# Kernel optimization log

Measured on AMD Instinct MI355X. Metric: run time of the kernel, lower is better.

## Reference

```python
import jax, jax.numpy as jnp
import numpy as np

DT = 0.5
NE, NIN = 400, 784
# excitatory LIF
THRESH_E, OFFSET, VRESET_E, EREST_E, REFRAC_E, TAU_MEM_E = -52.0, 20.0, -65.0, -65.0, 5.0, 100.0
# inhibitory LIF
THRESH_I, VRESET_I, EREST_I, REFRAC_I, TAU_MEM_I = -40.0, -45.0, -60.0, 2.0, 10.0
# synapses
TAU_SYN_E, TAU_SYN_I = 1.0, 2.0
E_EI, E_IE, E_EE = 0.0, -100.0, 0.0
# STDP
TC_P1, TC_P2, TC_PRE = 20.0, 40.0, 20.0
NU_PRE, NU_POST, WMAX = 0.0001, 0.01, 1.0
THETA0 = 20.0


def lif_step(mem, rc, I, thresh, v_reset, erest, tau, refrac):
    # conductance-based LIF with refractory period (inferred LIFei semantics)
    active = rc <= 0.0
    mem = jnp.where(active, mem + (erest - mem + I) * (DT / tau), mem)
    rc = jnp.maximum(rc - DT, 0.0)
    spike = (active & (mem > thresh)).astype(mem.dtype)
    fired = spike > 0.0
    mem = jnp.where(fired, v_reset, mem)
    rc = jnp.where(fired, refrac, rc)
    return mem, rc, spike


def setup_inputs() -> dict:
    key = jax.random.key(0)
    k1, k2 = jax.random.split(key)
    x = jax.random.uniform(k1, (50, 512, NIN), dtype=jnp.float32)  # Poisson-rate encoded frames
    W_ine = (jax.random.uniform(k2, (NE, NIN), dtype=jnp.float32) + 0.01) * 0.3  # create_ine
    W_ei = jnp.eye(NE, dtype=jnp.float32) * 10.4                                  # create_ei
    W_ie = (jnp.ones((NE, NE), jnp.float32) - jnp.eye(NE, dtype=jnp.float32)) * 17.0  # create_ie
    return {"x": x, "W_ine": W_ine, "W_ei": W_ei, "W_ie": W_ie}


def reference(x, W_ine, W_ei, W_ie):
    T, B, _ = x.shape
    z_e = jnp.zeros((B, NE), x.dtype)

    def step(carry, xt_t):
        xt, t = xt_t
        (W, g_ine, g_ei, g_ie, Iie, mem_e, rc_e, mem_i, rc_i,
         theta, tr_pre, tp1, tp2) = carry
        # normweight: rows sum to 78.4
        W = W / (jnp.sum(W, axis=1, keepdims=True) / 78.4)
        # input -> e synapse (STDP-plastic)
        dg_ine = xt @ W.T                         # (B, NE)
        I_ine = g_ine * (E_EE - mem_e)            # g=0 at t=0 -> I=0 (matches None init)
        g_ine = g_ine + (dg_ine - g_ine) * (DT / TAU_SYN_E)
        # excitatory LIF with adaptive threshold
        thr_e = THRESH_E - OFFSET + theta
        mem_e, rc_e, spike_e = lif_step(mem_e, rc_e, I_ine + Iie, thr_e,
                                        VRESET_E, EREST_E, TAU_MEM_E, REFRAC_E)
        # e -> i synapse
        dg_ei = spike_e @ W_ei.T
        I_ei = g_ei * (E_EI - mem_i)
        g_ei = g_ei + (dg_ei - g_ei) * (DT / TAU_SYN_E)
        # inhibitory LIF
        mem_i, rc_i, spike_i = lif_step(mem_i, rc_i, I_ei, THRESH_I,
                                        VRESET_I, EREST_I, TAU_MEM_I, REFRAC_I)
        # i -> e synapse (current fed into NEXT step's lif_e)
        dg_ie = spike_i @ W_ie.T
        Iie = g_ie * (E_IE - mem_e)
        g_ie = g_ie + (dg_ie - g_ie) * (DT / TAU_SYN_I)
        # threshold homeostasis
        theta = theta * (1.0 - DT / 1e7) + 0.05 * spike_e
        # pre trace: first call copies x, later decay then set to 1 where x>0.9
        tr_pre_upd = jnp.where(xt > 0.9, 1.0, tr_pre * (1.0 - DT / TC_PRE))
        tr_pre = jnp.where(t == 0, xt, tr_pre_upd)
        # post traces: return decayed value, then set to 1 where spike
        ret1 = tp1 * (1.0 - DT / TC_P1)
        ret2 = tp2 * (1.0 - DT / TC_P2)
        fired = spike_e > 0.9
        tp1 = jnp.where(fired, 1.0, ret1)
        tp2 = jnp.where(fired, 1.0, ret2)
        # STDP: autograd.grad of dg=x@W^T w.r.t. W with grad_outputs G is G^T @ x
        dw = (NU_PRE * jnp.einsum('be,bi->ei', ret1, xt)
              + NU_POST * jnp.einsum('be,bi->ei', spike_e * ret2, tr_pre))
        W = jnp.clip(W + dw, 0.0, WMAX)
        new_carry = (W, g_ine, g_ei, g_ie, Iie, mem_e, rc_e, mem_i, rc_i,
                     theta, tr_pre, tp1, tp2)
        return new_carry, spike_e

    carry0 = (W_ine,
              z_e, z_e, z_e,                      # g_ine, g_ei, g_ie
              z_e,                                # Iie
              jnp.full((B, NE), EREST_E, x.dtype), z_e,   # mem_e, rc_e
              jnp.full((B, NE), EREST_I, x.dtype), z_e,   # mem_i, rc_i
              jnp.full((B, NE), THETA0, x.dtype),         # theta
              jnp.zeros((B, NIN), x.dtype),               # trace_pre
              z_e, z_e)                                   # trace_post1/2
    _, spikes = jax.lax.scan(step, carry0, (x, jnp.arange(T)))
    return spikes  # (T, B, NE)
```

## Files before the change

kernel.cpp:

```cpp
#include <hip/hip_runtime.h>

#define NE 400
#define NIN 784
#define BB 512
#define TT 50

#define KC1 14
#define KCH1 56
#define KT1 8
#define KC2 16
#define KCH2 64

constexpr float C_KE     = (float)(0.5 / 100.0);
constexpr float C_KI     = (float)(0.5 / 10.0);
constexpr float C_GSE    = 0.5f;
constexpr float C_GSI    = 0.25f;
constexpr float C_DECTH  = (float)(1.0 - 0.5 / 1e7);
constexpr float C_DEC1   = (float)(1.0 - 0.5 / 20.0);
constexpr float C_DEC2   = (float)(1.0 - 0.5 / 40.0);
constexpr float C_DECPRE = (float)(1.0 - 0.5 / 20.0);
constexpr float C_NUPRE  = (float)0.0001;
constexpr float C_NUPOST = 0.01f;

__global__ void k_init(float* g_ine, float* g_ei, float* g_ie, float* Iie,
                       float* mem_e, float* rc_e, float* mem_i, float* rc_i,
                       float* theta, float* tp1, float* tp2) {
    int i = blockIdx.x * blockDim.x + threadIdx.x;
    if (i < BB * NE) {
        g_ine[i] = 0.f; g_ei[i] = 0.f; g_ie[i] = 0.f; Iie[i] = 0.f;
        mem_e[i] = -65.0f; rc_e[i] = 0.f;
        mem_i[i] = -60.0f; rc_i[i] = 0.f;
        theta[i] = 20.0f; tp1[i] = 0.f; tp2[i] = 0.f;
    }
}

__global__ __launch_bounds__(256) void k_pre(const float* __restrict__ W,
                                             float* __restrict__ d,
                                             const float* __restrict__ x0,
                                             float* __restrict__ tr) {
    int bid = blockIdx.x, tid = threadIdx.x;
    if (bid >= NE) {
        int base = (bid - NE) * 2048 + tid * 4;
        *(float4*)&tr[base] = *(const float4*)&x0[base];
        return;
    }
    __shared__ float red[256];
    float s = 0.f;
    if (tid < 196) {
        float4 w = *(const float4*)&W[bid * NIN + tid * 4];
        s = w.x + w.y + w.z + w.w;
    }
    red[tid] = s;
    __syncthreads();
    for (int off = 128; off > 0; off >>= 1) {
        if (tid < off) red[tid] += red[tid + off];
        __syncthreads();
    }
    if (tid == 0) d[bid] = red[0] / 78.4f;
}

__global__ __launch_bounds__(256) void k_g1(const float* __restrict__ x,
                                            const float* __restrict__ W,
                                            float* __restrict__ dgp) {
    __shared__ float sA[KT1][68];
    __shared__ float sB[KT1][132];
    const int lid = threadIdx.x;
    const int tx = lid & 15, ty = lid >> 4;
    const int e0 = blockIdx.x * 128, b0 = blockIdx.y * 64;
    const int kb = blockIdx.z * KCH1;
    const int xr = lid >> 2, xc = (lid & 3) * 2;
    const int wr = lid >> 1, wc = (lid & 1) * 4;
    const bool wv_ok = (e0 + wr) < NE;
    const float4 z4 = make_float4(0.f, 0.f, 0.f, 0.f);

    float acc[4][2][4];
#pragma unroll
    for (int p = 0; p < 4; p++)
#pragma unroll
        for (int h = 0; h < 2; h++)
#pragma unroll
            for (int q = 0; q < 4; q++) acc[p][h][q] = 0.f;

    float2 xv;
    float4 wv;
    auto ld = [&](int kt) {
        int k0 = kb + kt * KT1;
        xv = *(const float2*)&x[(b0 + xr) * NIN + k0 + xc];
        wv = wv_ok ? *(const float4*)&W[(e0 + wr) * NIN + k0 + wc] : z4;
    };

    ld(0);
    for (int kt = 0; kt < KCH1 / KT1; kt++) {
        sA[xc + 0][xr] = xv.x; sA[xc + 1][xr] = xv.y;
        sB[wc + 0][wr] = wv.x; sB[wc + 1][wr] = wv.y;
        sB[wc + 2][wr] = wv.z; sB[wc + 3][wr] = wv.w;
        __syncthreads();
        if (kt < KCH1 / KT1 - 1) ld(kt + 1);
#pragma unroll
        for (int k = 0; k < KT1; k++) {
            float4 av = *(const float4*)&sA[k][ty * 4];
            float4 b0v = *(const float4*)&sB[k][tx * 4];
            float4 b1v = *(const float4*)&sB[k][64 + tx * 4];
            float a[4] = {av.x, av.y, av.z, av.w};
            float bq0[4] = {b0v.x, b0v.y, b0v.z, b0v.w};
            float bq1[4] = {b1v.x, b1v.y, b1v.z, b1v.w};
#pragma unroll
            for (int p = 0; p < 4; p++)
#pragma unroll
                for (int q = 0; q < 4; q++) {
                    acc[p][0][q] += a[p] * bq0[q];
                    acc[p][1][q] += a[p] * bq1[q];
                }
        }
        __syncthreads();
    }
    float* basep = dgp + (size_t)blockIdx.z * BB * NE;
    int c1 = e0 + tx * 4, c2 = e0 + 64 + tx * 4;
#pragma unroll
    for (int p = 0; p < 4; p++) {
        int row = b0 + ty * 4 + p;
        if (c1 < NE)
            *(float4*)&basep[row * NE + c1] =
                make_float4(acc[p][0][0], acc[p][0][1], acc[p][0][2], acc[p][0][3]);
        if (c2 < NE)
            *(float4*)&basep[row * NE + c2] =
                make_float4(acc[p][1][0], acc[p][1][1], acc[p][1][2], acc[p][1][3]);
    }
}

__global__ __launch_bounds__(512) void k_mid(const float* __restrict__ dgp,
                                             const float* __restrict__ d,
                                             float* g_ine, float* g_ei, float* g_ie,
                                             float* Iie, float* mem_e, float* rc_e,
                                             float* mem_i, float* rc_i, float* theta,
                                             float* tp1, float* tp2,
                                             float* __restrict__ A1s,
                                             float* __restrict__ A2s,
                                             float* __restrict__ out_t) {
    int b = blockIdx.x;
    int e = threadIdx.x;
    __shared__ float red[8];
    int idx = b * NE + e;

    float spk_i = 0.f, spk_e = 0.f;
    float g1 = 0.f, me = 0.f, re = 0.f, th = 0.f, g2 = 0.f, mi = 0.f, ri = 0.f;

    if (e < NE) {
        float dg = 0.f;
#pragma unroll
        for (int c = 0; c < KC1; c++) dg += dgp[(size_t)c * BB * NE + idx];
        dg = dg / d[e];
        g1 = g_ine[idx]; me = mem_e[idx]; re = rc_e[idx];
        th = theta[idx];
        float Ii = Iie[idx];
        float I_in = g1 * (0.0f - me);
        g1 = g1 + (dg - g1) * C_GSE;
        bool act = (re <= 0.0f);
        float I = I_in + Ii;
        if (act) me = me + ((-65.0f - me) + I) * C_KE;
        re = fmaxf(re - 0.5f, 0.0f);
        float thr = -72.0f + th;
        spk_e = (act && (me > thr)) ? 1.0f : 0.0f;
        if (spk_e > 0.0f) { me = -65.0f; re = 5.0f; }
        float dgei = spk_e * 10.4f;
        g2 = g_ei[idx]; mi = mem_i[idx]; ri = rc_i[idx];
        float I_ei = g2 * (0.0f - mi);
        g2 = g2 + (dgei - g2) * C_GSE;
        bool ai = (ri <= 0.0f);
        if (ai) mi = mi + ((-60.0f - mi) + I_ei) * C_KI;
        ri = fmaxf(ri - 0.5f, 0.0f);
        spk_i = (ai && (mi > -40.0f)) ? 1.0f : 0.0f;
        if (spk_i > 0.0f) { mi = -45.0f; ri = 2.0f; }
    }
    float v = spk_i;
#pragma unroll
    for (int o = 32; o > 0; o >>= 1) v += __shfl_down(v, o, 64);
    if ((e & 63) == 0) red[e >> 6] = v;
    __syncthreads();
    float S = ((red[0] + red[1]) + (red[2] + red[3])) +
              ((red[4] + red[5]) + (red[6] + red[7]));
    if (e < NE) {
        float dgie = 17.0f * (S - spk_i);
        float g3 = g_ie[idx];
        float Iie_new = g3 * (-100.0f - me);
        g3 = g3 + (dgie - g3) * C_GSI;
        float th2 = th * C_DECTH + 0.05f * spk_e;
        float r1 = tp1[idx] * C_DEC1;
        float r2 = tp2[idx] * C_DEC2;
        bool fired = spk_e > 0.9f;
        A1s[idx] = C_NUPRE * r1;
        A2s[idx] = C_NUPOST * (spk_e * r2);
        tp1[idx] = fired ? 1.0f : r1;
        tp2[idx] = fired ? 1.0f : r2;
        g_ine[idx] = g1; g_ei[idx] = g2; g_ie[idx] = g3; Iie[idx] = Iie_new;
        mem_e[idx] = me; rc_e[idx] = re; mem_i[idx] = mi; rc_i[idx] = ri;
        theta[idx] = th2;
        out_t[idx] = spk_e;
    }
}

__global__ __launch_bounds__(256) void k_g2(const float* __restrict__ A1s,
                                            const float* __restrict__ A2s,
                                            const float* __restrict__ x,
                                            const float* __restrict__ tr,
                                            float* __restrict__ part) {
    __shared__ float sA[16][68];
    __shared__ float sB[16][132];
    const int lid = threadIdx.x;
    const int tx = lid & 15, ty = lid >> 4;
    const int e0 = blockIdx.x * 64, i0 = blockIdx.y * 128;
    const int kb = blockIdx.z * KCH2;
    const int kr = lid >> 4;
    const int jc = (lid & 15) * 4;
    const float4 z4 = make_float4(0.f, 0.f, 0.f, 0.f);

    float acc[4][2][4];
#pragma unroll
    for (int p = 0; p < 4; p++)
#pragma unroll
        for (int h = 0; h < 2; h++)
#pragma unroll
            for (int q = 0; q < 4; q++) acc[p][h][q] = 0.f;

    float4 av_, bv0_, bv1_;
    auto ld = [&](int kt) {
        int gb = kb + kt * 16 + kr;
        int ec = e0 + jc;
        if (ec < NE)
            av_ = (gb < BB) ? *(const float4*)&A1s[gb * NE + ec]
                            : *(const float4*)&A2s[(gb - BB) * NE + ec];
        else av_ = z4;
        const float* src; int rb;
        if (gb < BB) { src = x; rb = gb; } else { src = tr; rb = gb - BB; }
        int c1 = i0 + jc, c2 = i0 + 64 + jc;
        bv0_ = (c1 < NIN) ? *(const float4*)&src[rb * NIN + c1] : z4;
        bv1_ = (c2 < NIN) ? *(const float4*)&src[rb * NIN + c2] : z4;
    };

    ld(0);
    for (int kt = 0; kt < KCH2 / 16; kt++) {
        *(float4*)&sA[kr][jc] = av_;
        *(float4*)&sB[kr][jc] = bv0_;
        *(float4*)&sB[kr][64 + jc] = bv1_;
        __syncthreads();
        if (kt < KCH2 / 16 - 1) ld(kt + 1);
#pragma unroll
        for (int k = 0; k < 16; k++) {
            float4 av = *(const float4*)&sA[k][ty * 4];
            float4 b0v = *(const float4*)&sB[k][tx * 4];
            float4 b1v = *(const float4*)&sB[k][64 + tx * 4];
            float a[4] = {av.x, av.y, av.z, av.w};
            float bq0[4] = {b0v.x, b0v.y, b0v.z, b0v.w};
            float bq1[4] = {b1v.x, b1v.y, b1v.z, b1v.w};
#pragma unroll
            for (int p = 0; p < 4; p++)
#pragma unroll
                for (int q = 0; q < 4; q++) {
                    acc[p][0][q] += a[p] * bq0[q];
                    acc[p][1][q] += a[p] * bq1[q];
                }
        }
        __syncthreads();
    }
    float* basep = part + (size_t)blockIdx.z * NE * NIN;
    int c1 = i0 + tx * 4, c2 = i0 + 64 + tx * 4;
#pragma unroll
    for (int p = 0; p < 4; p++) {
        int row = e0 + ty * 4 + p;
        if (row < NE) {
            if (c1 < NIN)
                *(float4*)&basep[row * NIN + c1] =
                    make_float4(acc[p][0][0], acc[p][0][1], acc[p][0][2], acc[p][0][3]);
            if (c2 < NIN)
                *(float4*)&basep[row * NIN + c2] =
                    make_float4(acc[p][1][0], acc[p][1][1], acc[p][1][2], acc[p][1][3]);
        }
    }
}

__global__ __launch_bounds__(256) void k_wup(float* __restrict__ W,
                                             const float* __restrict__ part,
                                             float* __restrict__ d,
                                             const float* __restrict__ x1,
                                             float* __restrict__ tr) {
    int bid = blockIdx.x, tid = threadIdx.x;
    if (bid >= NE) {
        int base = (bid - NE) * 2048 + tid * 4;
        float4 xv = *(const float4*)&x1[base];
        float4 tv = *(const float4*)&tr[base];
        float4 o;
        o.x = (xv.x > 0.9f) ? 1.f : tv.x * C_DECPRE;
        o.y = (xv.y > 0.9f) ? 1.f : tv.y * C_DECPRE;
        o.z = (xv.z > 0.9f) ? 1.f : tv.z * C_DECPRE;
        o.w = (xv.w > 0.9f) ? 1.f : tv.w * C_DECPRE;
        *(float4*)&tr[base] = o;
        return;
    }
    __shared__ float red[256];
    float dv = d[bid];
    float s = 0.f;
    if (tid < 196) {
        int off = bid * NIN + tid * 4;
        float4 w = *(const float4*)&W[off];
        float4 acc = make_float4(w.x / dv, w.y / dv, w.z / dv, w.w / dv);
#pragma unroll
        for (int c = 0; c < KC2; c++) {
            float4 p = *(const float4*)&part[(size_t)c * NE * NIN + off];
            acc.x += p.x; acc.y += p.y; acc.z += p.z; acc.w += p.w;
        }
        acc.x = fminf(fmaxf(acc.x, 0.f), 1.f);
        acc.y = fminf(fmaxf(acc.y, 0.f), 1.f);
        acc.z = fminf(fmaxf(acc.z, 0.f), 1.f);
        acc.w = fminf(fmaxf(acc.w, 0.f), 1.f);
        *(float4*)&W[off] = acc;
        s = acc.x + acc.y + acc.z + acc.w;
    }
    red[tid] = s;
    __syncthreads();
    for (int off = 128; off > 0; off >>= 1) {
        if (tid < off) red[tid] += red[tid + off];
        __syncthreads();
    }
    if (tid == 0) d[bid] = red[0] / 78.4f;
}

extern "C" void kernel_launch(void* const* d_in, const int* in_sizes, int n_in,
                              void* d_out, int out_size, void* d_ws, size_t ws_size,
                              hipStream_t stream) {
    const float* x     = (const float*)d_in[0];
    const float* W_ine = (const float*)d_in[1];

    float* p = (float*)d_ws;
    float* W_cur = p; p += NE * NIN;
    float* dbuf  = p; p += NE;
    float* dgp   = p; p += (size_t)KC1 * BB * NE;
    float* part  = p; p += (size_t)KC2 * NE * NIN;
    float* A1s   = p; p += BB * NE;
    float* A2s   = p; p += BB * NE;
    float* g_ine = p; p += BB * NE;
    float* g_ei  = p; p += BB * NE;
    float* g_ie  = p; p += BB * NE;
    float* Iie   = p; p += BB * NE;
    float* mem_e = p; p += BB * NE;
    float* rc_e  = p; p += BB * NE;
    float* mem_i = p; p += BB * NE;
    float* rc_i  = p; p += BB * NE;
    float* theta = p; p += BB * NE;
    float* tp1   = p; p += BB * NE;
    float* tp2   = p; p += BB * NE;
    float* tr    = p; p += BB * NIN;

    hipMemcpyAsync(W_cur, W_ine, (size_t)NE * NIN * sizeof(float),
                   hipMemcpyDeviceToDevice, stream);
    k_init<<<(BB * NE + 255) / 256, 256, 0, stream>>>(g_ine, g_ei, g_ie, Iie, mem_e,
                                                      rc_e, mem_i, rc_i, theta, tp1, tp2);
    k_pre<<<NE + 196, 256, 0, stream>>>(W_cur, dbuf, x, tr);

    for (int t = 0; t < TT; t++) {
        const float* xt = x + (size_t)t * BB * NIN;
        float* out_t = (float*)d_out + (size_t)t * BB * NE;
        k_g1<<<dim3(4, 8, KC1), 256, 0, stream>>>(xt, W_cur, dgp);
        k_mid<<<BB, 512, 0, stream>>>(dgp, dbuf, g_ine, g_ei, g_ie,
                                      Iie, mem_e, rc_e, mem_i, rc_i, theta,
                                      tp1, tp2, A1s, A2s, out_t);
        if (t < TT - 1) {
            k_g2<<<dim3(7, 7, KC2), 256, 0, stream>>>(A1s, A2s, xt, tr, part);
            k_wup<<<NE + 196, 256, 0, stream>>>(W_cur, part, dbuf,
                                                xt + (size_t)BB * NIN, tr);
        }
    }
}
```

Measured before the change: 2.098 ms.

## Fuse weight update into STDP GEMM via last-block atomic, fold trace update into k_g1

Removes the separate k_wup kernel. The last-arriving split-K block of each 64x128 patch (detected with an atomic counter and threadfence) reduces the partials, clips W and writes per-patch row sums. k_mid then derives the normalisation divisor from those row sums. The pre-trace decay moves into extra blocks of k_g1, and the init, copy and normalisation kernels merge into one. The split-K factor for the dW GEMM is halved, and both GEMMs gain double-buffered shared memory, with k_g1 retiled to 128x64. This cuts launches and global round-trips, at the cost of serialised tail work in the last block of each patch and fewer parallel blocks in k_g2f.

Result: slower. 5.384 ms (+156.6%).

```diff
diff --git a/kernel.cpp b/kernel.cpp
--- a/kernel.cpp
+++ b/kernel.cpp
@@ -8,8 +8,9 @@
 #define KC1 14
 #define KCH1 56
 #define KT1 8
-#define KC2 16
-#define KCH2 64
+#define KC2 8
+#define KCH2 128
+#define NPATCH 49
 
 constexpr float C_KE     = (float)(0.5 / 100.0);
 constexpr float C_KI     = (float)(0.5 / 10.0);
@@ -22,114 +23,158 @@
 constexpr float C_NUPRE  = (float)0.0001;
 constexpr float C_NUPOST = 0.01f;
 
-__global__ void k_init(float* g_ine, float* g_ei, float* g_ie, float* Iie,
-                       float* mem_e, float* rc_e, float* mem_i, float* rc_i,
-                       float* theta, float* tp1, float* tp2) {
-    int i = blockIdx.x * blockDim.x + threadIdx.x;
-    if (i < BB * NE) {
+template <bool USE_PARTS>
+__device__ __forceinline__ void patch_update(const float* __restrict__ Wsrc,
+                                             float* __restrict__ Wdst,
+                                             const float* __restrict__ part,
+                                             const float* __restrict__ dbuf,
+                                             float* __restrict__ rs,
+                                             int ex, int iy, int lid) {
+    int e_l = lid >> 2, lg = lid & 3;
+    int e = ex * 64 + e_l;
+    float rsum = 0.f;
+    if (e < NE) {
+        float dv = USE_PARTS ? dbuf[e] : 1.0f;
+#pragma unroll
+        for (int j8 = 0; j8 < 8; j8++) {
+            int f4 = iy * 32 + lg * 8 + j8;
+            if (f4 < 196) {
+                int off = e * NIN + f4 * 4;
+                float4 w = *(const float4*)&Wsrc[off];
+                float4 a = make_float4(w.x / dv, w.y / dv, w.z / dv, w.w / dv);
+                if (USE_PARTS) {
+#pragma unroll
+                    for (int c = 0; c < KC2; c++) {
+                        float4 pp = *(const float4*)&part[(size_t)c * NE * NIN + off];
+                        a.x += pp.x; a.y += pp.y; a.z += pp.z; a.w += pp.w;
+                    }
+                }
+                a.x = fminf(fmaxf(a.x, 0.f), 1.f);
+                a.y = fminf(fmaxf(a.y, 0.f), 1.f);
+                a.z = fminf(fmaxf(a.z, 0.f), 1.f);
+                a.w = fminf(fmaxf(a.w, 0.f), 1.f);
+                *(float4*)&Wdst[off] = a;
+                rsum += (a.x + a.y) + (a.z + a.w);
+            }
+        }
+    }
+    float v = rsum;
+    v += __shfl_down(v, 2, 64);
+    v += __shfl_down(v, 1, 64);
+    if (lg == 0 && e < NE) rs[iy * NE + e] = v;
+}
+
+__global__ __launch_bounds__(256) void k_init(const float* __restrict__ W0,
+                                              float* __restrict__ W,
+                                              float* __restrict__ rs,
+                                              int* __restrict__ cnt,
+                                              const float* __restrict__ x0,
+                                              float* __restrict__ tr,
+                                              float* g_ine, float* g_ei, float* g_ie,
+                                              float* Iie, float* mem_e, float* rc_e,
+                                              float* mem_i, float* rc_i, float* theta,
+                                              float* tp1, float* tp2) {
+    int bid = blockIdx.x, lid = threadIdx.x;
+    if (bid < 800) {
+        int i = bid * 256 + lid;
         g_ine[i] = 0.f; g_ei[i] = 0.f; g_ie[i] = 0.f; Iie[i] = 0.f;
         mem_e[i] = -65.0f; rc_e[i] = 0.f;
         mem_i[i] = -60.0f; rc_i[i] = 0.f;
         theta[i] = 20.0f; tp1[i] = 0.f; tp2[i] = 0.f;
-    }
-}
-
-__global__ __launch_bounds__(256) void k_pre(const float* __restrict__ W,
-                                             float* __restrict__ d,
-                                             const float* __restrict__ x0,
-                                             float* __restrict__ tr) {
-    int bid = blockIdx.x, tid = threadIdx.x;
-    if (bid >= NE) {
-        int base = (bid - NE) * 2048 + tid * 4;
+        if (bid == 0 && lid < NPATCH) cnt[lid] = 0;
+    } else if (bid < 800 + NPATCH) {
+        int pid = bid - 800;
+        patch_update<false>(W0, W, nullptr, nullptr, rs, pid / 7, pid % 7, lid);
+    } else {
+        int base = (bid - 800 - NPATCH) * 2048 + lid * 4;
         *(float4*)&tr[base] = *(const float4*)&x0[base];
-        return;
-    }
-    __shared__ float red[256];
-    float s = 0.f;
-    if (tid < 196) {
-        float4 w = *(const float4*)&W[bid * NIN + tid * 4];
-        s = w.x + w.y + w.z + w.w;
-    }
-    red[tid] = s;
-    __syncthreads();
-    for (int off = 128; off > 0; off >>= 1) {
-        if (tid < off) red[tid] += red[tid + off];
-        __syncthreads();
-    }
-    if (tid == 0) d[bid] = red[0] / 78.4f;
+    }
 }
 
 __global__ __launch_bounds__(256) void k_g1(const float* __restrict__ x,
                                             const float* __restrict__ W,
-                                            float* __restrict__ dgp) {
-    __shared__ float sA[KT1][68];
-    __shared__ float sB[KT1][132];
+                                            float* __restrict__ dgp,
+                                            float* __restrict__ tr, int t) {
+    __shared__ float sA[2][KT1][132];
+    __shared__ float sB[2][KT1][68];
     const int lid = threadIdx.x;
+    int j = blockIdx.x;
+    if (j >= 392) {
+        if (t == 0) return;
+        int base = (j - 392) * 2048 + lid * 4;
+        float4 xv = *(const float4*)&x[base];
+        float4 tv = *(const float4*)&tr[base];
+        float4 o;
+        o.x = (xv.x > 0.9f) ? 1.f : tv.x * C_DECPRE;
+        o.y = (xv.y > 0.9f) ? 1.f : tv.y * C_DECPRE;
+        o.z = (xv.z > 0.9f) ? 1.f : tv.z * C_DECPRE;
+        o.w = (xv.w > 0.9f) ? 1.f : tv.w * C_DECPRE;
+        *(float4*)&tr[base] = o;
+        return;
+    }
+    const int kz = j / 28, rem = j % 28;
+    const int by = rem / 7, ex = rem % 7;
+    const int e0 = ex * 64, b0 = by * 128, kb = kz * KCH1;
     const int tx = lid & 15, ty = lid >> 4;
-    const int e0 = blockIdx.x * 128, b0 = blockIdx.y * 64;
-    const int kb = blockIdx.z * KCH1;
-    const int xr = lid >> 2, xc = (lid & 3) * 2;
-    const int wr = lid >> 1, wc = (lid & 1) * 4;
-    const bool wv_ok = (e0 + wr) < NE;
-    const float4 z4 = make_float4(0.f, 0.f, 0.f, 0.f);
-
-    float acc[4][2][4];
-#pragma unroll
-    for (int p = 0; p < 4; p++)
-#pragma unroll
-        for (int h = 0; h < 2; h++)
-#pragma unroll
-            for (int q = 0; q < 4; q++) acc[p][h][q] = 0.f;
-
-    float2 xv;
-    float4 wv;
+    const int xr = lid >> 1, xc = (lid & 1) * 4;
+    const int wr = lid >> 2, wc = (lid & 3) * 2;
+    const bool wok = (e0 + wr) < NE;
+
+    float acc[8][4];
+#pragma unroll
+    for (int p = 0; p < 8; p++)
+#pragma unroll
+        for (int q = 0; q < 4; q++) acc[p][q] = 0.f;
+
+    float4 xv;
+    float2 wv;
     auto ld = [&](int kt) {
         int k0 = kb + kt * KT1;
-        xv = *(const float2*)&x[(b0 + xr) * NIN + k0 + xc];
-        wv = wv_ok ? *(const float4*)&W[(e0 + wr) * NIN + k0 + wc] : z4;
+        xv = *(const float4*)&x[(b0 + xr) * NIN + k0 + xc];
+        wv = wok ? *(const float2*)&W[(e0 + wr) * NIN + k0 + wc]
+                 : make_float2(0.f, 0.f);
     };
-
-    ld(0);
-    for (int kt = 0; kt < KCH1 / KT1; kt++) {
-        sA[xc + 0][xr] = xv.x; sA[xc + 1][xr] = xv.y;
-        sB[wc + 0][wr] = wv.x; sB[wc + 1][wr] = wv.y;
-        sB[wc + 2][wr] = wv.z; sB[wc + 3][wr] = wv.w;
+    auto st = [&](int buf) {
+        sA[buf][xc + 0][xr] = xv.x; sA[buf][xc + 1][xr] = xv.y;
+        sA[buf][xc + 2][xr] = xv.z; sA[buf][xc + 3][xr] = xv.w;
+        sB[buf][wc + 0][wr] = wv.x; sB[buf][wc + 1][wr] = wv.y;
+    };
+
+    ld(0); st(0);
+    __syncthreads();
+    const int NKT = KCH1 / KT1;
+    for (int kt = 0; kt < NKT; kt++) {
+        int cur = kt & 1;
+        if (kt + 1 < NKT) ld(kt + 1);
+#pragma unroll
+        for (int k = 0; k < KT1; k++) {
+            float4 a0 = *(const float4*)&sA[cur][k][ty * 8];
+            float4 a1 = *(const float4*)&sA[cur][k][ty * 8 + 4];
+            float4 bv = *(const float4*)&sB[cur][k][tx * 4];
+            float a[8] = {a0.x, a0.y, a0.z, a0.w, a1.x, a1.y, a1.z, a1.w};
+            float b[4] = {bv.x, bv.y, bv.z, bv.w};
+#pragma unroll
+            for (int p = 0; p < 8; p++)
+#pragma unroll
+                for (int q = 0; q < 4; q++) acc[p][q] += a[p] * b[q];
+        }
+        if (kt + 1 < NKT) st(cur ^ 1);
         __syncthreads();
-        if (kt < KCH1 / KT1 - 1) ld(kt + 1);
-#pragma unroll
-        for (int k = 0; k < KT1; k++) {
-            float4 av = *(const float4*)&sA[k][ty * 4];
-            float4 b0v = *(const float4*)&sB[k][tx * 4];
-            float4 b1v = *(const float4*)&sB[k][64 + tx * 4];
-            float a[4] = {av.x, av.y, av.z, av.w};
-            float bq0[4] = {b0v.x, b0v.y, b0v.z, b0v.w};
-            float bq1[4] = {b1v.x, b1v.y, b1v.z, b1v.w};
-#pragma unroll
-            for (int p = 0; p < 4; p++)
-#pragma unroll
-                for (int q = 0; q < 4; q++) {
-                    acc[p][0][q] += a[p] * bq0[q];
-                    acc[p][1][q] += a[p] * bq1[q];
-                }
-        }
-        __syncthreads();
-    }
-    float* basep = dgp + (size_t)blockIdx.z * BB * NE;
-    int c1 = e0 + tx * 4, c2 = e0 + 64 + tx * 4;
-#pragma unroll
-    for (int p = 0; p < 4; p++) {
-        int row = b0 + ty * 4 + p;
-        if (c1 < NE)
-            *(float4*)&basep[row * NE + c1] =
-                make_float4(acc[p][0][0], acc[p][0][1], acc[p][0][2], acc[p][0][3]);
-        if (c2 < NE)
-            *(float4*)&basep[row * NE + c2] =
-                make_float4(acc[p][1][0], acc[p][1][1], acc[p][1][2], acc[p][1][3]);
+    }
+    if (e0 + tx * 4 < NE) {
+        float* basep = dgp + (size_t)kz * BB * NE;
+#pragma unroll
+        for (int p = 0; p < 8; p++) {
+            int row = b0 + ty * 8 + p;
+            *(float4*)&basep[row * NE + e0 + tx * 4] =
+                make_float4(acc[p][0], acc[p][1], acc[p][2], acc[p][3]);
+        }
     }
 }
 
 __global__ __launch_bounds__(512) void k_mid(const float* __restrict__ dgp,
-                                             const float* __restrict__ d,
+                                             const float* __restrict__ rs,
+                                             float* __restrict__ dbuf,
                                              float* g_ine, float* g_ei, float* g_ie,
                                              float* Iie, float* mem_e, float* rc_e,
                                              float* mem_i, float* rc_i, float* theta,
@@ -146,10 +191,15 @@
     float g1 = 0.f, me = 0.f, re = 0.f, th = 0.f, g2 = 0.f, mi = 0.f, ri = 0.f;
 
     if (e < NE) {
+        float dsum = 0.f;
+#pragma unroll
+        for (int iy = 0; iy < 7; iy++) dsum += rs[iy * NE + e];
+        float dv = dsum / 78.4f;
+        if (b == 0) dbuf[e] = dv;
         float dg = 0.f;
 #pragma unroll
         for (int c = 0; c < KC1; c++) dg += dgp[(size_t)c * BB * NE + idx];
-        dg = dg / d[e];
+        dg = dg / dv;
         g1 = g_ine[idx]; me = mem_e[idx]; re = rc_e[idx];
         th = theta[idx];
         float Ii = Iie[idx];
@@ -199,16 +249,21 @@
     }
 }
 
-__global__ __launch_bounds__(256) void k_g2(const float* __restrict__ A1s,
-                                            const float* __restrict__ A2s,
-                                            const float* __restrict__ x,
-                                            const float* __restrict__ tr,
-                                            float* __restrict__ part) {
-    __shared__ float sA[16][68];
-    __shared__ float sB[16][132];
+__global__ __launch_bounds__(256) void k_g2f(const float* __restrict__ A1s,
+                                             const float* __restrict__ A2s,
+                                             const float* __restrict__ x,
+                                             const float* __restrict__ tr,
+                                             float* __restrict__ part,
+                                             float* __restrict__ W,
+                                             const float* __restrict__ dbuf,
+                                             float* __restrict__ rs,
+                                             int* __restrict__ cnt) {
+    __shared__ float sA[2][16][68];
+    __shared__ float sB[2][16][132];
     const int lid = threadIdx.x;
     const int tx = lid & 15, ty = lid >> 4;
-    const int e0 = blockIdx.x * 64, i0 = blockIdx.y * 128;
+    const int ex = blockIdx.x, iy = blockIdx.y;
+    const int e0 = ex * 64, i0 = iy * 128;
     const int kb = blockIdx.z * KCH2;
     const int kr = lid >> 4;
     const int jc = (lid & 15) * 4;
@@ -225,30 +280,33 @@
     float4 av_, bv0_, bv1_;
     auto ld = [&](int kt) {
         int gb = kb + kt * 16 + kr;
-        int ec = e0 + jc;
-        if (ec < NE)
-            av_ = (gb < BB) ? *(const float4*)&A1s[gb * NE + ec]
-                            : *(const float4*)&A2s[(gb - BB) * NE + ec];
-        else av_ = z4;
+        av_ = (e0 + jc < NE)
+                  ? ((gb < BB) ? *(const float4*)&A1s[gb * NE + e0 + jc]
+                               : *(const float4*)&A2s[(gb - BB) * NE + e0 + jc])
+                  : z4;
         const float* src; int rb;
         if (gb < BB) { src = x; rb = gb; } else { src = tr; rb = gb - BB; }
         int c1 = i0 + jc, c2 = i0 + 64 + jc;
         bv0_ = (c1 < NIN) ? *(const float4*)&src[rb * NIN + c1] : z4;
         bv1_ = (c2 < NIN) ? *(const float4*)&src[rb * NIN + c2] : z4;
     };
-
-    ld(0);
-    for (int kt = 0; kt < KCH2 / 16; kt++) {
-        *(float4*)&sA[kr][jc] = av_;
-        *(float4*)&sB[kr][jc] = bv0_;
-        *(float4*)&sB[kr][64 + jc] = bv1_;
-        __syncthreads();
-        if (kt < KCH2 / 16 - 1) ld(kt + 1);
+    auto st = [&](int buf) {
+        *(float4*)&sA[buf][kr][jc] = av_;
+        *(float4*)&sB[buf][kr][jc] = bv0_;
+        *(float4*)&sB[buf][kr][64 + jc] = bv1_;
+    };
+
+    ld(0); st(0);
+    __syncthreads();
+    const int NKT = KCH2 / 16;
+    for (int kt = 0; kt < NKT; kt++) {
+        int cur = kt & 1;
+        if (kt + 1 < NKT) ld(kt + 1);
 #pragma unroll
         for (int k = 0; k < 16; k++) {
-            float4 av = *(const float4*)&sA[k][ty * 4];
-            float4 b0v = *(const float4*)&sB[k][tx * 4];
-            float4 b1v = *(const float4*)&sB[k][64 + tx * 4];
+            float4 av = *(const float4*)&sA[cur][k][ty * 4];
+            float4 b0v = *(const float4*)&sB[cur][k][tx * 4];
+            float4 b1v = *(const float4*)&sB[cur][k][64 + tx * 4];
             float a[4] = {av.x, av.y, av.z, av.w};
             float bq0[4] = {b0v.x, b0v.y, b0v.z, b0v.w};
             float bq1[4] = {b1v.x, b1v.y, b1v.z, b1v.w};
@@ -260,68 +318,35 @@
                     acc[p][1][q] += a[p] * bq1[q];
                 }
         }
+        if (kt + 1 < NKT) st(cur ^ 1);
         __syncthreads();
     }
-    float* basep = part + (size_t)blockIdx.z * NE * NIN;
-    int c1 = i0 + tx * 4, c2 = i0 + 64 + tx * 4;
-#pragma unroll
-    for (int p = 0; p < 4; p++) {
-        int row = e0 + ty * 4 + p;
-        if (row < NE) {
-            if (c1 < NIN)
-                *(float4*)&basep[row * NIN + c1] =
-                    make_float4(acc[p][0][0], acc[p][0][1], acc[p][0][2], acc[p][0][3]);
-            if (c2 < NIN)
-                *(float4*)&basep[row * NIN + c2] =
-                    make_float4(acc[p][1][0], acc[p][1][1], acc[p][1][2], acc[p][1][3]);
-        }
-    }
-}
-
-__global__ __launch_bounds__(256) void k_wup(float* __restrict__ W,
-                                             const float* __restrict__ part,
-                                             float* __restrict__ d,
-                                             const float* __restrict__ x1,
-                                             float* __restrict__ tr) {
-    int bid = blockIdx.x, tid = threadIdx.x;
-    if (bid >= NE) {
-        int base = (bid - NE) * 2048 + tid * 4;
-        float4 xv = *(const float4*)&x1[base];
-        float4 tv = *(const float4*)&tr[base];
-        float4 o;
-        o.x = (xv.x > 0.9f) ? 1.f : tv.x * C_DECPRE;
-        o.y = (xv.y > 0.9f) ? 1.f : tv.y * C_DECPRE;
-        o.z = (xv.z > 0.9f) ? 1.f : tv.z * C_DECPRE;
-        o.w = (xv.w > 0.9f) ? 1.f : tv.w * C_DECPRE;
-        *(float4*)&tr[base] = o;
-        return;
-    }
-    __shared__ float red[256];
-    float dv = d[bid];
-    float s = 0.f;
-    if (tid < 196) {
-        int off = bid * NIN + tid * 4;
-        float4 w = *(const float4*)&W[off];
-        float4 acc = make_float4(w.x / dv, w.y / dv, w.z / dv, w.w / dv);
-#pragma unroll
-        for (int c = 0; c < KC2; c++) {
-            float4 p = *(const float4*)&part[(size_t)c * NE * NIN + off];
-            acc.x += p.x; acc.y += p.y; acc.z += p.z; acc.w += p.w;
-        }
-        acc.x = fminf(fmaxf(acc.x, 0.f), 1.f);
-        acc.y = fminf(fmaxf(acc.y, 0.f), 1.f);
-        acc.z = fminf(fmaxf(acc.z, 0.f), 1.f);
-        acc.w = fminf(fmaxf(acc.w, 0.f), 1.f);
-        *(float4*)&W[off] = acc;
-        s = acc.x + acc.y + acc.z + acc.w;
-    }
-    red[tid] = s;
-    __syncthreads();
-    for (int off = 128; off > 0; off >>= 1) {
-        if (tid < off) red[tid] += red[tid + off];
-        __syncthreads();
-    }
-    if (tid == 0) d[bid] = red[0] / 78.4f;
+    {
+        float* basep = part + (size_t)blockIdx.z * NE * NIN;
+        int c1 = i0 + tx * 4, c2 = i0 + 64 + tx * 4;
+#pragma unroll
+        for (int p = 0; p < 4; p++) {
+            int row = e0 + ty * 4 + p;
+            if (row < NE) {
+                if (c1 < NIN)
+                    *(float4*)&basep[row * NIN + c1] = make_float4(
+                        acc[p][0][0], acc[p][0][1], acc[p][0][2], acc[p][0][3]);
+                if (c2 < NIN)
+                    *(float4*)&basep[row * NIN + c2] = make_float4(
+                        acc[p][1][0], acc[p][1][1], acc[p][1][2], acc[p][1][3]);
+            }
+        }
+    }
+    __threadfence();
+    __syncthreads();
+    __shared__ int lastf;
+    int patch = ex * 7 + iy;
+    if (lid == 0) lastf = (atomicAdd(&cnt[patch], 1) == KC2 - 1) ? 1 : 0;
+    __syncthreads();
+    if (!lastf) return;
+    __threadfence();
+    patch_update<true>(W, W, part, dbuf, rs, ex, iy, lid);
+    if (lid == 0) cnt[patch] = 0;
 }
 
 extern "C" void kernel_launch(void* const* d_in, const int* in_sizes, int n_in,
@@ -333,6 +358,8 @@
     float* p = (float*)d_ws;
     float* W_cur = p; p += NE * NIN;
     float* dbuf  = p; p += NE;
+    float* rs    = p; p += 7 * NE;
+    int*   cnt   = (int*)p; p += 64;
     float* dgp   = p; p += (size_t)KC1 * BB * NE;
     float* part  = p; p += (size_t)KC2 * NE * NIN;
     float* A1s   = p; p += BB * NE;
@@ -350,23 +377,19 @@
     float* tp2   = p; p += BB * NE;
     float* tr    = p; p += BB * NIN;
 
-    hipMemcpyAsync(W_cur, W_ine, (size_t)NE * NIN * sizeof(float),
-                   hipMemcpyDeviceToDevice, stream);
-    k_init<<<(BB * NE + 255) / 256, 256, 0, stream>>>(g_ine, g_ei, g_ie, Iie, mem_e,
-                                                      rc_e, mem_i, rc_i, theta, tp1, tp2);
-    k_pre<<<NE + 196, 256, 0, stream>>>(W_cur, dbuf, x, tr);
+    k_init<<<800 + NPATCH + 196, 256, 0, stream>>>(W_ine, W_cur, rs, cnt, x, tr,
+                                                   g_ine, g_ei, g_ie, Iie, mem_e,
+                                                   rc_e, mem_i, rc_i, theta, tp1, tp2);
 
     for (int t = 0; t < TT; t++) {
         const float* xt = x + (size_t)t * BB * NIN;
         float* out_t = (float*)d_out + (size_t)t * BB * NE;
-        k_g1<<<dim3(4, 8, KC1), 256, 0, stream>>>(xt, W_cur, dgp);
-        k_mid<<<BB, 512, 0, stream>>>(dgp, dbuf, g_ine, g_ei, g_ie,
+        k_g1<<<588, 256, 0, stream>>>(xt, W_cur, dgp, tr, t);
+        k_mid<<<BB, 512, 0, stream>>>(dgp, rs, dbuf, g_ine, g_ei, g_ie,
                                       Iie, mem_e, rc_e, mem_i, rc_i, theta,
                                       tp1, tp2, A1s, A2s, out_t);
-        if (t < TT - 1) {
-            k_g2<<<dim3(7, 7, KC2), 256, 0, stream>>>(A1s, A2s, xt, tr, part);
-            k_wup<<<NE + 196, 256, 0, stream>>>(W_cur, part, dbuf,
-                                                xt + (size_t)BB * NIN, tr);
-        }
-    }
-}
+        if (t < TT - 1)
+            k_g2f<<<dim3(7, 7, KC2), 256, 0, stream>>>(A1s, A2s, xt, tr, part,
+                                                       W_cur, dbuf, rs, cnt);
+    }
+}
```
